# Performance work log

Hardware: AMD Instinct MI355X
Metric: run time of the kernel (lower is better)

## Reference

```python
import jax, jax.numpy as jnp
import numpy as np

B, SD, SE, DM, H, DK, DV, DFF = 4, 2048, 2048, 1024, 8, 128, 128, 4096
NEG = -jnp.inf


def _linear(x, w, b):
    # torch nn.Linear: w [out, in]
    return jnp.einsum('...i,oi->...o', x, w) + b


def _layer_norm(x, g, b, eps=1e-5):
    mu = jnp.mean(x, axis=-1, keepdims=True)
    var = jnp.var(x, axis=-1, keepdims=True)
    return (x - mu) * jax.lax.rsqrt(var + eps) * g + b


def _mha(Q, K, V, wq, bq, wk, bk, wv, bv, wo, bo, pad_mask, seq_mask):
    # wq/wk: [H, DK, DM], wv: [H, DV, DM]; vectorized over the per-head Linears
    Qh = jnp.einsum('bsd,hkd->bhsk', Q, wq) + bq[None, :, None, :]  # [B,H,Sq,DK]
    Kh = jnp.einsum('bsd,hkd->bhsk', K, wk) + bk[None, :, None, :]  # [B,H,Sk,DK]
    Vh = jnp.einsum('bsd,hvd->bhsv', V, wv) + bv[None, :, None, :]  # [B,H,Sk,DV]
    scores = jnp.einsum('bhqd,bhkd->bhqk', Qh, Kh) / np.sqrt(DK)
    scores = jnp.where(pad_mask[:, None, :, :] == 0, NEG, scores)
    if seq_mask is not None:
        scores = jnp.where(seq_mask[None, None, :, :] == 0, NEG, scores)
    w = jax.nn.softmax(scores, axis=-1)
    out = jnp.einsum('bhqk,bhkv->bhqv', w, Vh)  # [B,H,Sq,DV]
    out = out.transpose(0, 2, 1, 3).reshape(Q.shape[0], Q.shape[1], H * DV)
    return _linear(out, wo, bo)


def setup_inputs() -> dict:
    key = jax.random.key(0)
    ks = iter(jax.random.split(key, 40))
    s = 0.02
    d = {
        'output_embs': jax.random.normal(next(ks), (B, SD, DM), jnp.float32),
        'encoder_output': jax.random.normal(next(ks), (B, SE, DM), jnp.float32),
        'inputs_padding_mask': jnp.ones((B, 1, SE), jnp.int32),
        'outputs_padding_mask': jnp.ones((B, 1, SD), jnp.int32),
    }
    for name in ['q1', 'k1', 'v1', 'q2', 'k2', 'v2']:
        d[name + '_w'] = jax.random.normal(next(ks), (DM, DM), jnp.float32) * s
        d[name + '_b'] = jnp.zeros((DM,), jnp.float32)
    for p in ['sa', 'ed']:
        d[p + '_qw'] = jax.random.normal(next(ks), (H, DK, DM), jnp.float32) * s
        d[p + '_qb'] = jnp.zeros((H, DK), jnp.float32)
        d[p + '_kw'] = jax.random.normal(next(ks), (H, DK, DM), jnp.float32) * s
        d[p + '_kb'] = jnp.zeros((H, DK), jnp.float32)
        d[p + '_vw'] = jax.random.normal(next(ks), (H, DV, DM), jnp.float32) * s
        d[p + '_vb'] = jnp.zeros((H, DV), jnp.float32)
        d[p + '_ow'] = jax.random.normal(next(ks), (DM, H * DV), jnp.float32) * s
        d[p + '_ob'] = jnp.zeros((DM,), jnp.float32)
    d['ff_w1'] = jax.random.normal(next(ks), (DFF, DM), jnp.float32) * s
    d['ff_b1'] = jnp.zeros((DFF,), jnp.float32)
    d['ff_w2'] = jax.random.normal(next(ks), (DM, DFF), jnp.float32) * s
    d['ff_b2'] = jnp.zeros((DM,), jnp.float32)
    d['ln1_g'] = jnp.ones((DM,), jnp.float32)
    d['ln1_b'] = jnp.zeros((DM,), jnp.float32)
    d['ln2_g'] = jnp.ones((DM,), jnp.float32)
    d['ln2_b'] = jnp.zeros((DM,), jnp.float32)
    return d


def reference(output_embs, encoder_output, inputs_padding_mask, outputs_padding_mask,
              q1_w, q1_b, k1_w, k1_b, v1_w, v1_b,
              q2_w, q2_b, k2_w, k2_b, v2_w, v2_b,
              sa_qw, sa_qb, sa_kw, sa_kb, sa_vw, sa_vb, sa_ow, sa_ob,
              ed_qw, ed_qb, ed_kw, ed_kb, ed_vw, ed_vb, ed_ow, ed_ob,
              ff_w1, ff_b1, ff_w2, ff_b2, ln1_g, ln1_b, ln2_g, ln2_b):
    # Dropout (p=0.1 in torch) treated as identity for a deterministic reference.
    seq_len = output_embs.shape[1]
    seq_mask = jnp.tril(jnp.ones((seq_len, seq_len), jnp.float32))
    Q = _linear(output_embs, q1_w, q1_b)
    K = _linear(output_embs, k1_w, k1_b)
    V = _linear(output_embs, v1_w, v1_b)
    x = output_embs + _mha(Q, K, V, sa_qw, sa_qb, sa_kw, sa_kb, sa_vw, sa_vb,
                           sa_ow, sa_ob, outputs_padding_mask, seq_mask)
    x = _layer_norm(x, ln1_g, ln1_b)
    Q2 = _linear(x, q2_w, q2_b)
    K2 = _linear(encoder_output, k2_w, k2_b)
    V2 = _linear(encoder_output, v2_w, v2_b)
    # NOTE: original adds residual from output_embs (not x) -- kept faithful.
    y = output_embs + _mha(Q2, K2, V2, ed_qw, ed_qb, ed_kw, ed_kb, ed_vw, ed_vb,
                           ed_ow, ed_ob, inputs_padding_mask, None)
    y = _layer_norm(y, ln2_g, ln2_b)
    ff = _linear(jax.nn.relu(_linear(y, ff_w1, ff_b1)), ff_w2, ff_b2)
    out = y + ff
    # original reuses layer_norm2 for the final norm (layer_norm3 unused) -- faithful.
    out = _layer_norm(out, ln2_g, ln2_b)
    return out
```

## Files before the change

### kernel.cpp

```cpp
#include <hip/hip_runtime.h>
#include <hip/hip_bf16.h>

typedef __hip_bfloat16 bf16;
typedef short short8 __attribute__((ext_vector_type(8)));
typedef short short4v __attribute__((ext_vector_type(4)));
typedef float floatx4 __attribute__((ext_vector_type(4)));
typedef int intx4 __attribute__((ext_vector_type(4)));
typedef unsigned int uintx4 __attribute__((ext_vector_type(4)));

#define B_ 4
#define SD_ 2048
#define SE_ 2048
#define DM_ 1024
#define H_ 8
#define DFF_ 4096

struct PtrsIn  { const void* p[6]; };
struct PtrsOut { void* p[6]; };
struct Int6    { int v[6]; };

__device__ __forceinline__ float b2f(bf16 v) { return __bfloat162float(v); }
__device__ __forceinline__ bf16 f2b(float v) { return __float2bfloat16(v); }
__device__ __forceinline__ short f2s(float v) { return __builtin_bit_cast(short, __float2bfloat16(v)); }

__device__ __forceinline__ unsigned cvtpk_bf16(float lo, float hi) {
    unsigned r;
    asm("v_cvt_pk_bf16_f32 %0, %1, %2" : "=v"(r) : "v"(lo), "v"(hi));
    return r;
}
__device__ __forceinline__ void pl32swap(unsigned &x, unsigned &y) {
    asm("v_permlane32_swap_b32 %0, %1" : "+v"(x), "+v"(y));
}
__device__ __forceinline__ void pl16swap(unsigned &x, unsigned &y) {
    asm("v_permlane16_swap_b32 %0, %1" : "+v"(x), "+v"(y));
}

__device__ __forceinline__ void gl_lds16(const short* g, short* l) {
    __builtin_amdgcn_global_load_lds(
        (const __attribute__((address_space(1))) void*)g,
        (__attribute__((address_space(3))) void*)l, 16, 0, 0);
}

__global__ __launch_bounds__(256) void cvt6(PtrsIn in, PtrsOut out, Int6 n)
{
    const int y = blockIdx.y;
    int i = (blockIdx.x * 256 + threadIdx.x) * 8;
    if (i >= n.v[y]) return;
    const float* src = (const float*)in.p[y];
    bf16* dst = (bf16*)out.p[y];
    floatx4 a = *(const floatx4*)(src + i);
    floatx4 b = *(const floatx4*)(src + i + 4);
    short8 r;
#pragma unroll
    for (int k = 0; k < 4; ++k) { r[k] = f2s(a[k]); r[k + 4] = f2s(b[k]); }
    *(short8*)(dst + i) = r;
}

__global__ __launch_bounds__(256) void cvtT6(PtrsIn in, bf16* out)
{
    __shared__ short tl[32][36];
    const int z = blockIdx.z;
    const float* src = (const float*)in.p[z];
    bf16* dst = out + (size_t)z * 1024 * 1024;
    const int tid = threadIdx.x;
    const int i = tid >> 3;
    const int j = (tid & 7) * 4;
    const int r0 = blockIdx.x * 32, c0 = blockIdx.y * 32;
    floatx4 v = *(const floatx4*)(src + (size_t)(r0 + i) * 1024 + c0 + j);
#pragma unroll
    for (int p = 0; p < 4; ++p) tl[i][j + p] = f2s(v[p]);
    __syncthreads();
    short4v r;
#pragma unroll
    for (int p = 0; p < 4; ++p) r[p] = tl[j + p][i];
    *(short4v*)(dst + (size_t)(c0 + i) * 1024 + r0 + j) = r;
}

__global__ __launch_bounds__(256) void bias6(
    PtrsIn w6, PtrsIn bin6, PtrsIn badd6, PtrsOut out6)
{
    __shared__ float red[4];
    const int y = blockIdx.y;
    const float* w    = (const float*)w6.p[y];
    const float* bin  = (const float*)bin6.p[y];
    const float* badd = (const float*)badd6.p[y];
    float* out        = (float*)out6.p[y];
    const int o = blockIdx.x;
    const int t = threadIdx.x;
    float s = 0.f;
#pragma unroll
    for (int i = t; i < 1024; i += 256) s += w[(size_t)o * 1024 + i] * bin[i];
#pragma unroll
    for (int off = 32; off >= 1; off >>= 1) s += __shfl_xor(s, off);
    if ((t & 63) == 0) red[t >> 6] = s;
    __syncthreads();
    if (t == 0) out[o] = red[0] + red[1] + red[2] + red[3] + badd[o];
}

__global__ __launch_bounds__(256) void gemm_prep(PtrsIn A6, PtrsIn W6, PtrsOut C6)
{
    __shared__ __align__(16) short As[16 * 512];
    __shared__ __align__(16) short Ws[16 * 512];

    const int K = 1024, N = 1024;
    const int z = blockIdx.z;
    const bf16* A = (const bf16*)A6.p[z];
    const bf16* W = (const bf16*)W6.p[z];
    bf16* C = (bf16*)C6.p[z];

    const int tid  = threadIdx.x;
    const int lane = tid & 63;
    const int wave = tid >> 6;
    const int quad = lane >> 4;
    const int l16  = lane & 15;
    const int r7   = l16 & 7;
    const int bm0  = blockIdx.y * 128;
    const int bn0  = blockIdx.x * 128;
    const int wm   = (wave >> 1) * 64;
    const int wn   = (wave & 1) * 64;

    const int scol = (((lane & 7) ^ (lane >> 3)) * 8);
    const short* Ag = (const short*)A + (size_t)(bm0 + wave * 32 + (lane >> 3)) * K + scol;
    const short* Wg = (const short*)W + (size_t)(bn0 + wave * 32 + (lane >> 3)) * K + scol;
    short* Al = As + (wave * 4) * 512;
    short* Wl = Ws + (wave * 4) * 512;

    floatx4 acc[4][4];
#pragma unroll
    for (int i = 0; i < 4; ++i)
#pragma unroll
        for (int j = 0; j < 4; ++j)
            acc[i][j] = (floatx4){0.f, 0.f, 0.f, 0.f};

    for (int k0 = 0; k0 < K; k0 += 64) {
        __syncthreads();
#pragma unroll
        for (int s = 0; s < 4; ++s) {
            gl_lds16(Ag + k0 + (size_t)s * 8 * K, Al + s * 512);
            gl_lds16(Wg + k0 + (size_t)s * 8 * K, Wl + s * 512);
        }
        __syncthreads();
#pragma unroll
        for (int kk = 0; kk < 64; kk += 32) {
            short8 af[4], bg[4];
#pragma unroll
            for (int i = 0; i < 4; ++i) {
                int row = wm + i * 16 + l16;
                af[i] = *(const short8*)&As[(row >> 3) * 512 + r7 * 64 +
                                            (((quad + (kk >> 3)) ^ r7) << 3)];
            }
#pragma unroll
            for (int j = 0; j < 4; ++j) {
                int row = wn + j * 16 + l16;
                bg[j] = *(const short8*)&Ws[(row >> 3) * 512 + r7 * 64 +
                                            (((quad + (kk >> 3)) ^ r7) << 3)];
            }
#pragma unroll
            for (int i = 0; i < 4; ++i)
#pragma unroll
                for (int j = 0; j < 4; ++j)
                    acc[i][j] = __builtin_amdgcn_mfma_f32_16x16x32_bf16(
                        af[i], bg[j], acc[i][j], 0, 0, 0);
        }
    }

#pragma unroll
    for (int j = 0; j < 4; ++j) {
        int col = bn0 + wn + j * 16 + l16;
#pragma unroll
        for (int i = 0; i < 4; ++i) {
            int row0 = bm0 + wm + i * 16 + quad * 4;
#pragma unroll
            for (int r = 0; r < 4; ++r)
                C[(size_t)(row0 + r) * N + col] = f2b(acc[i][j][r]);
        }
    }
}

template <int RELU>
__global__ __launch_bounds__(512, 2) void gemm256(
    const bf16* __restrict__ A, const bf16* __restrict__ W,
    const float* __restrict__ bias, bf16* __restrict__ C,
    int M, int N, int K)
{
    __shared__ __align__(16) short L[3 * 24576];

    const int tid  = threadIdx.x;
    const int lane = tid & 63;
    const int wave = tid >> 6;
    const int quad = lane >> 4;
    const int l16  = lane & 15;
    const int r7   = l16 & 7;
    const int wm   = wave >> 1;
    const int wn   = wave & 1;

    const int gx  = gridDim.x;
    const int nwg = gx * gridDim.y;
    int wg = blockIdx.y * gx + blockIdx.x;
    if ((nwg & 7) == 0) wg = (wg & 7) * (nwg >> 3) + (wg >> 3);
    const int bn0 = (wg % gx) * 128;
    const int bm0 = (wg / gx) * 256;

    const int scol = (((lane & 7) ^ ((lane >> 3) & 7)) * 8);
    const short* Ag = (const short*)A + (size_t)(bm0 + wave * 32 + (lane >> 3)) * K + scol;
    const short* Wg = (const short*)W + (size_t)(bn0 + wave * 16 + (lane >> 3)) * K + scol;
    const int aw = (wave * 32) * 64;
    const int bw = 16384 + (wave * 16) * 64;

    floatx4 acc[4][4];
#pragma unroll
    for (int i = 0; i < 4; ++i)
#pragma unroll
        for (int j = 0; j < 4; ++j)
            acc[i][j] = (floatx4){0.f, 0.f, 0.f, 0.f};

    const int T = K / 64;

#pragma unroll
    for (int i = 0; i < 4; ++i) gl_lds16(Ag + (size_t)(i * 8) * K, L + aw + i * 8 * 64);
#pragma unroll
    for (int i = 0; i < 2; ++i) gl_lds16(Wg + (size_t)(i * 8) * K, L + bw + i * 8 * 64);
#pragma unroll
    for (int i = 0; i < 4; ++i) gl_lds16(Ag + 64 + (size_t)(i * 8) * K, L + 24576 + aw + i * 8 * 64);
#pragma unroll
    for (int i = 0; i < 2; ++i) gl_lds16(Wg + 64 + (size_t)(i * 8) * K, L + 24576 + bw + i * 8 * 64);
    asm volatile("s_waitcnt vmcnt(6)" ::: "memory");
    __builtin_amdgcn_s_barrier();

    int cur = 0, stg = 2;
    for (int t = 0; t < T; ++t) {
        __builtin_amdgcn_sched_barrier(0);
        const int kt = (t + 2 < T) ? (t + 2) : (T - 1);
        const size_t kg = (size_t)kt * 64;
        const short* Ac = L + cur * 24576;
        const short* Bc = Ac + 16384;
        short* As_s = L + stg * 24576 + aw;
        short* Bs_s = L + stg * 24576 + bw;

        short8 af[2][2], bf[4][2];

#pragma unroll
        for (int mi = 0; mi < 2; ++mi)
#pragma unroll
            for (int ks = 0; ks < 2; ++ks)
                af[mi][ks] = *(const short8*)&Ac[(wm * 64 + mi * 16 + l16) * 64 +
                                                (((ks * 4 + quad) ^ r7) << 3)];
#pragma unroll
        for (int nf = 0; nf < 4; ++nf)
#pragma unroll
            for (int ks = 0; ks < 2; ++ks)
                bf[nf][ks] = *(const short8*)&Bc[(wn * 64 + nf * 16 + l16) * 64 +
                                                (((ks * 4 + quad) ^ r7) << 3)];
        gl_lds16(Ag + kg, As_s);
        gl_lds16(Ag + kg + (size_t)8 * K, As_s + 8 * 64);
        gl_lds16(Wg + kg, Bs_s);
        __builtin_amdgcn_s_barrier();
        asm volatile("s_waitcnt lgkmcnt(0)" ::: "memory");
        __builtin_amdgcn_sched_barrier(0);
        __builtin_amdgcn_s_setprio(1);
#pragma unroll
        for (int ks = 0; ks < 2; ++ks)
#pragma unroll
            for (int mi = 0; mi < 2; ++mi)
#pragma unroll
                for (int nf = 0; nf < 4; ++nf)
                    acc[mi][nf] = __builtin_amdgcn_mfma_f32_16x16x32_bf16(
                        af[mi][ks], bf[nf][ks], acc[mi][nf], 0, 0, 0);
        __builtin_amdgcn_s_setprio(0);
        __builtin_amdgcn_s_barrier();

#pragma unroll
        for (int mi = 0; mi < 2; ++mi)
#pragma unroll
            for (int ks = 0; ks < 2; ++ks)
                af[mi][ks] = *(const short8*)&Ac[(wm * 64 + (2 + mi) * 16 + l16) * 64 +
                                                (((ks * 4 + quad) ^ r7) << 3)];
        gl_lds16(Ag + kg + (size_t)16 * K, As_s + 16 * 64);
        gl_lds16(Ag + kg + (size_t)24 * K, As_s + 24 * 64);
        gl_lds16(Wg + kg + (size_t)8 * K, Bs_s + 8 * 64);
        __builtin_amdgcn_s_barrier();
        asm volatile("s_waitcnt lgkmcnt(0)" ::: "memory");
        __builtin_amdgcn_sched_barrier(0);
        __builtin_amdgcn_s_setprio(1);
#pragma unroll
        for (int ks = 0; ks < 2; ++ks)
#pragma unroll
            for (int mi = 0; mi < 2; ++mi)
#pragma unroll
                for (int nf = 0; nf < 4; ++nf)
                    acc[2 + mi][nf] = __builtin_amdgcn_mfma_f32_16x16x32_bf16(
                        af[mi][ks], bf[nf][ks], acc[2 + mi][nf], 0, 0, 0);
        __builtin_amdgcn_s_setprio(0);
        asm volatile("s_waitcnt vmcnt(6)" ::: "memory");
        __builtin_amdgcn_s_barrier();

        cur = (cur == 2) ? 0 : cur + 1;
        stg = (stg == 2) ? 0 : stg + 1;
    }

#pragma unroll
    for (int nf = 0; nf < 4; ++nf) {
        int col = bn0 + wn * 64 + nf * 16 + l16;
        float bv = bias ? bias[col] : 0.f;
#pragma unroll
        for (int mf = 0; mf < 4; ++mf) {
            int row0 = bm0 + wm * 64 + mf * 16 + quad * 4;
#pragma unroll
            for (int r = 0; r < 4; ++r) {
                float v = acc[mf][nf][r] + bv;
                if (RELU) v = fmaxf(v, 0.f);
                C[(size_t)(row0 + r) * N + col] = f2b(v);
            }
        }
    }
}

__global__ __launch_bounds__(256) void vtrans(
    const bf16* __restrict__ in, int str, bf16* __restrict__ out, int S)
{
    __shared__ short t[32][36];
    const int tid = threadIdx.x;
    const int s0  = blockIdx.x * 32;
    const int d0  = blockIdx.y * 32;
    const int bh  = blockIdx.z;
    const int b = bh >> 3, h = bh & 7;
    const int i = tid >> 3;
    const int j = (tid & 7) * 4;

    *(short4v*)&t[i][j] =
        *(const short4v*)(in + (size_t)(b * S + s0 + i) * str + h * 128 + d0 + j);
    __syncthreads();
    short4v r;
#pragma unroll
    for (int p = 0; p < 4; ++p) r[p] = t[j + p][i];
    *(short4v*)(out + ((size_t)bh * 128 + d0 + i) * S + s0 + j) = r;
}

template <int CAUSAL>
__global__ __launch_bounds__(256) void flash_attn(
    const bf16* __restrict__ Q, int qstr, const bf16* __restrict__ K, int kstr,
    const bf16* __restrict__ Vt, const int* __restrict__ pad,
    bf16* __restrict__ Of, float* __restrict__ Ls, int Sq, int Sk)
{
    __shared__ __align__(16) short Ks[64 * 128];
    __shared__ __align__(16) short Vs[128 * 64];

    const int tid  = threadIdx.x;
    const int lane = tid & 63;
    const int wave = tid >> 6;
    const int quad = lane >> 4;
    const int l16  = lane & 15;
    const int r7   = l16 & 7;
    const int bh   = blockIdx.x;
    const int b    = bh >> 3;
    const int h    = bh & 7;
    const int par  = blockIdx.y;
    const int tz   = blockIdx.z;

    const int NT = Sq >> 7;
    const float sc = 0.08838834764831845f * 1.4426950408889634f;
    const bf16* vb0 = Vt + (size_t)bh * 128 * Sk;
    const short* Kb = (const short*)K + (size_t)b * Sk * kstr + h * 128;

    int krr[4], kgg[4], vrr[4], vgg[4];
#pragma unroll
    for (int s = 0; s < 4; ++s) {
        int seg = wave * 4 + s;
        krr[s] = seg * 4 + (lane >> 4);
        kgg[s] = (l16 ^ (krr[s] & 7)) * 8;
        vrr[s] = seg * 8 + (lane >> 3);
        vgg[s] = ((lane & 7) ^ (vrr[s] & 7)) * 8;
    }

    const int npass = CAUSAL ? 2 : 1;
    for (int ps = 0; ps < npass; ++ps) {
        const int tile = CAUSAL ? (ps ? NT - 1 - tz : tz) : tz;
        const int q0 = tile * 128;
        const int qw = q0 + wave * 32;

        short8 qf[2][4];
#pragma unroll
        for (int mi = 0; mi < 2; ++mi) {
            const bf16* qb = Q + (size_t)(b * Sq + qw + mi * 16 + l16) * qstr + h * 128;
#pragma unroll
            for (int c = 0; c < 4; ++c)
                qf[mi][c] = *(const short8*)(qb + c * 32 + quad * 8);
        }

        floatx4 o[2][8];
#pragma unroll
        for (int mi = 0; mi < 2; ++mi)
#pragma unroll
            for (int nf = 0; nf < 8; ++nf) o[mi][nf] = (floatx4){0.f, 0.f, 0.f, 0.f};
        float lsum[2] = {0.f, 0.f};

        int kEnd = Sk;
        if (CAUSAL && q0 + 128 < Sk) kEnd = q0 + 128;

        intx4 sk[4], sv[4];
        {
            const int kc = par * 64;
#pragma unroll
            for (int s = 0; s < 4; ++s) {
                sk[s] = *(const intx4*)(Kb + (size_t)(kc + krr[s]) * kstr + kgg[s]);
                sv[s] = *(const intx4*)((const short*)vb0 + (size_t)vrr[s] * Sk + kc + vgg[s]);
            }
        }

        for (int ci = par; ci * 64 < kEnd; ci += 2) {
            const int kc = ci * 64;
            __syncthreads();
#pragma unroll
            for (int s = 0; s < 4; ++s) {
                *(intx4*)&Ks[(wave * 4 + s) * 512 + lane * 8] = sk[s];
                *(intx4*)&Vs[(wave * 4 + s) * 512 + lane * 8] = sv[s];
            }
            __syncthreads();

            const int kcn = kc + 128;
            if (kcn < kEnd) {
#pragma unroll
                for (int s = 0; s < 4; ++s) {
                    sk[s] = *(const intx4*)(Kb + (size_t)(kcn + krr[s]) * kstr + kgg[s]);
                    sv[s] = *(const intx4*)((const short*)vb0 + (size_t)vrr[s] * Sk + kcn + vgg[s]);
                }
            }
            __builtin_amdgcn_sched_barrier(0);

            short8 pfm[2][2];
#pragma unroll
            for (int c = 0; c < 2; ++c) {
                floatx4 sT[2][2];
#pragma unroll
                for (int fp = 0; fp < 2; ++fp) {
                    const int f = c * 2 + fp;
                    const int krow = f * 16 + l16;
                    short8 kf[4];
#pragma unroll
                    for (int cc = 0; cc < 4; ++cc)
                        kf[cc] = *(const short8*)&Ks[krow * 128 + (((cc * 4 + quad) ^ r7) << 3)];
#pragma unroll
                    for (int mi = 0; mi < 2; ++mi) {
                        floatx4 s = (floatx4){0.f, 0.f, 0.f, 0.f};
#pragma unroll
                        for (int cc = 0; cc < 4; ++cc)
                            s = __builtin_amdgcn_mfma_f32_16x16x32_bf16(
                                kf[cc], qf[mi][cc], s, 0, 0, 0);
                        sT[mi][fp] = s;
                    }
                }

                const int* pb = pad + (size_t)b * Sk + kc + c * 32 + quad * 4;
                intx4 pv0 = *(const intx4*)pb;
                intx4 pv1 = *(const intx4*)(pb + 16);

#pragma unroll
                for (int mi = 0; mi < 2; ++mi) {
                    const int qv = qw + mi * 16 + l16;
#pragma unroll
                    for (int fp = 0; fp < 2; ++fp) {
#pragma unroll
                        for (int r = 0; r < 4; ++r) {
                            int kk = kc + (c * 2 + fp) * 16 + quad * 4 + r;
                            bool ok = ((fp ? pv1[r] : pv0[r]) != 0);
                            if (CAUSAL) ok = ok && (kk <= qv);
                            float p = ok ? __builtin_amdgcn_exp2f(sT[mi][fp][r] * sc) : 0.f;
                            sT[mi][fp][r] = p;
                            lsum[mi] += p;
                        }
                    }
                    unsigned wA = cvtpk_bf16(sT[mi][0][0], sT[mi][0][1]);
                    unsigned wB = cvtpk_bf16(sT[mi][0][2], sT[mi][0][3]);
                    unsigned wC = cvtpk_bf16(sT[mi][1][0], sT[mi][1][1]);
                    unsigned wD = cvtpk_bf16(sT[mi][1][2], sT[mi][1][3]);
                    pl32swap(wA, wC);
                    pl16swap(wA, wC);
                    pl32swap(wB, wD);
                    pl16swap(wB, wD);
                    uintx4 t;
                    t[0] = wA; t[1] = wB; t[2] = wC; t[3] = wD;
                    pfm[mi][c] = __builtin_bit_cast(short8, t);
                }
            }

            __builtin_amdgcn_s_setprio(1);
#pragma unroll
            for (int nf = 0; nf < 8; ++nf) {
                int vrow = nf * 16 + l16;
                short8 vf0 = *(const short8*)&Vs[vrow * 64 + ((quad ^ r7) << 3)];
                short8 vf1 = *(const short8*)&Vs[vrow * 64 + (((4 + quad) ^ r7) << 3)];
#pragma unroll
                for (int mi = 0; mi < 2; ++mi) {
                    o[mi][nf] = __builtin_amdgcn_mfma_f32_16x16x32_bf16(
                        pfm[mi][0], vf0, o[mi][nf], 0, 0, 0);
                    o[mi][nf] = __builtin_amdgcn_mfma_f32_16x16x32_bf16(
                        pfm[mi][1], vf1, o[mi][nf], 0, 0, 0);
                }
            }
            __builtin_amdgcn_s_setprio(0);
        }

        bf16* op = Of + (size_t)par * B_ * Sq * DM_;
        float* lp = Ls + (size_t)par * B_ * H_ * Sq;
#pragma unroll
        for (int mi = 0; mi < 2; ++mi) {
            float s = lsum[mi];
            s += __shfl_xor(s, 16);
            s += __shfl_xor(s, 32);
            if (lane < 16)
                lp[(size_t)bh * Sq + qw + mi * 16 + l16] = s;
#pragma unroll
            for (int nf = 0; nf < 8; ++nf)
#pragma unroll
                for (int r = 0; r < 4; ++r) {
                    int q = qw + mi * 16 + quad * 4 + r;
                    op[(size_t)(b * Sq + q) * DM_ + h * 128 + nf * 16 + l16] =
                        f2b(o[mi][nf][r]);
                }
        }
    }
}

__global__ __launch_bounds__(256) void attn_combine(
    const bf16* __restrict__ Of, const float* __restrict__ Ls,
    bf16* __restrict__ out)
{
    const int row = blockIdx.x;
    const int t = threadIdx.x;
    const int col = t * 4;
    const int h = col >> 7;
    const int b = row >> 11;
    const int q = row & (SD_ - 1);
    const size_t NV = (size_t)B_ * SD_ * DM_;
    const int idx = (b * H_ + h) * SD_ + q;
    float l = Ls[idx] + Ls[B_ * H_ * SD_ + idx];
    float inv = l > 0.f ? 1.f / l : 0.f;
    size_t base = (size_t)row * DM_ + col;
    short4v a0 = *(const short4v*)(Of + base);
    short4v a1 = *(const short4v*)(Of + NV + base);
    short4v r;
#pragma unroll
    for (int i = 0; i < 4; ++i)
        r[i] = f2s((b2f(__builtin_bit_cast(bf16, (short)a0[i])) +
                    b2f(__builtin_bit_cast(bf16, (short)a1[i]))) * inv);
    *(short4v*)(out + base) = r;
}

template <int A32, int O32>
__global__ __launch_bounds__(256) void add_ln(
    const void* __restrict__ Ap, const bf16* __restrict__ Bv,
    const float* __restrict__ g, const float* __restrict__ be,
    void* __restrict__ outp)
{
    const int D = DM_;
    __shared__ float red[8];
    const size_t row = blockIdx.x;
    const int t = threadIdx.x;

    float x[4];
    {
        float av[4];
        if (A32) {
            floatx4 a4 = *(const floatx4*)((const float*)Ap + row * D + t * 4);
#pragma unroll
            for (int i = 0; i < 4; ++i) av[i] = a4[i];
        } else {
            short4v a4 = *(const short4v*)((const bf16*)Ap + row * D + t * 4);
#pragma unroll
            for (int i = 0; i < 4; ++i)
                av[i] = b2f(__builtin_bit_cast(bf16, (short)a4[i]));
        }
        short4v b4 = *(const short4v*)(Bv + row * D + t * 4);
#pragma unroll
        for (int i = 0; i < 4; ++i)
            x[i] = av[i] + b2f(__builtin_bit_cast(bf16, (short)b4[i]));
    }
    float s = 0.f, s2 = 0.f;
#pragma unroll
    for (int i = 0; i < 4; ++i) { s += x[i]; s2 += x[i] * x[i]; }
#pragma unroll
    for (int off = 32; off >= 1; off >>= 1) {
        s  += __shfl_xor(s, off);
        s2 += __shfl_xor(s2, off);
    }
    const int wave = t >> 6;
    if ((t & 63) == 0) { red[wave] = s; red[4 + wave] = s2; }
    __syncthreads();
    s  = red[0] + red[1] + red[2] + red[3];
    s2 = red[4] + red[5] + red[6] + red[7];
    const float mu   = s * (1.f / D);
    const float var  = s2 * (1.f / D) - mu * mu;
    const float rstd = rsqrtf(var + 1e-5f);
#pragma unroll
    for (int i = 0; i < 4; ++i) {
        int idx = t * 4 + i;
        float v = (x[i] - mu) * rstd * g[idx] + be[idx];
        if (O32) ((float*)outp)[row * D + idx] = v;
        else     ((bf16*)outp)[row * D + idx] = f2b(v);
    }
}

extern "C" void kernel_launch(void* const* d_in, const int* in_sizes, int n_in,
                              void* d_out, int out_size, void* d_ws, size_t ws_size,
                              hipStream_t stream)
{
    const float* emb    = (const float*)d_in[0];
    const float* enc    = (const float*)d_in[1];
    const int*  in_pad  = (const int*)d_in[2];
    const int*  out_pad = (const int*)d_in[3];
    const float* q1_w = (const float*)d_in[4];  const float* q1_b = (const float*)d_in[5];
    const float* k1_w = (const float*)d_in[6];  const float* k1_b = (const float*)d_in[7];
    const float* v1_w = (const float*)d_in[8];  const float* v1_b = (const float*)d_in[9];
    const float* q2_w = (const float*)d_in[10]; const float* q2_b = (const float*)d_in[11];
    const float* k2_w = (const float*)d_in[12]; const float* k2_b = (const float*)d_in[13];
    const float* v2_w = (const float*)d_in[14]; const float* v2_b = (const float*)d_in[15];
    const float* sa_qw = (const float*)d_in[16]; const float* sa_qb = (const float*)d_in[17];
    const float* sa_kw = (const float*)d_in[18]; const float* sa_kb = (const float*)d_in[19];
    const float* sa_vw = (const float*)d_in[20]; const float* sa_vb = (const float*)d_in[21];
    const float* sa_ow = (const float*)d_in[22]; const float* sa_ob = (const float*)d_in[23];
    const float* ed_qw = (const float*)d_in[24]; const float* ed_qb = (const float*)d_in[25];
    const float* ed_kw = (const float*)d_in[26]; const float* ed_kb = (const float*)d_in[27];
    const float* ed_vw = (const float*)d_in[28]; const float* ed_vb = (const float*)d_in[29];
    const float* ed_ow = (const float*)d_in[30]; const float* ed_ob = (const float*)d_in[31];
    const float* ff_w1 = (const float*)d_in[32]; const float* ff_b1 = (const float*)d_in[33];
    const float* ff_w2 = (const float*)d_in[34]; const float* ff_b2 = (const float*)d_in[35];
    const float* ln1_g = (const float*)d_in[36]; const float* ln1_b = (const float*)d_in[37];
    const float* ln2_g = (const float*)d_in[38]; const float* ln2_b = (const float*)d_in[39];

    const int M = B_ * SD_;
    const size_t MM = (size_t)1024 * 1024;
    bf16* ws = (bf16*)d_ws;

    bf16* Wqkv = ws;
    bf16* Wkv  = ws + 3 * MM;
    bf16* Wq2  = ws + 5 * MM;
    bf16* Wso  = ws + 6 * MM;
    bf16* Weo  = ws + 7 * MM;
    bf16* Wf1  = ws + 8 * MM;
    bf16* Wf2  = ws + 12 * MM;
    float* bQKV = (float*)(ws + 16 * MM);
    float* bKV  = bQKV + 3072;
    float* bQ2  = bKV + 2048;
    float* Lsum = bQ2 + 2048;
    bf16* hw   = ws + 17 * MM;
    bf16* ft   = ws + 23 * MM;
    bf16* emb_b = ws + 17 * MM;
    bf16* enc_b = ws + 25 * MM;
    bf16* sqkv  = ws + 33 * MM;
    bf16* skv   = ws + 33 * MM;
    bf16* sq2   = ws + 49 * MM;
    bf16* sVt   = ws + 57 * MM;
    bf16* attn  = ws + 65 * MM;
    bf16* Ofb   = ws + 73 * MM;
    bf16* s1    = ws + 73 * MM;
    bf16* x     = ws + 89 * MM;
    bf16* y     = ws + 33 * MM;
    bf16* mid   = ws + 41 * MM;
    bf16* f2    = ws + 81 * MM;

    auto G = [&](const bf16* Ai, const bf16* Wi, const float* bi, bf16* Ci,
                 int Mi, int Ni, int Ki, bool relu) {
        dim3 grid(Ni / 128, Mi / 256);
        if (relu) gemm256<1><<<grid, 512, 0, stream>>>(Ai, Wi, bi, Ci, Mi, Ni, Ki);
        else      gemm256<0><<<grid, 512, 0, stream>>>(Ai, Wi, bi, Ci, Mi, Ni, Ki);
    };

    {
        PtrsIn in; PtrsOut out; Int6 n;
        const float* s6[6] = {sa_qw, sa_kw, sa_vw, ed_qw, ed_kw, ed_vw};
        for (int i = 0; i < 6; ++i) { in.p[i] = s6[i]; out.p[i] = hw + i * MM; n.v[i] = (int)MM; }
        cvt6<<<dim3(512, 6), 256, 0, stream>>>(in, out, n);
    }
    {
        PtrsIn in;
        const float* s6[6] = {q1_w, k1_w, v1_w, q2_w, k2_w, v2_w};
        for (int i = 0; i < 6; ++i) in.p[i] = s6[i];
        cvtT6<<<dim3(32, 32, 6), 256, 0, stream>>>(in, ft);
    }
    {
        PtrsIn A, W; PtrsOut C;
        const int idx[6] = {0, 1, 2, 4, 5, 3};
        bf16* c6[6] = {Wqkv, Wqkv + MM, Wqkv + 2 * MM, Wkv, Wkv + MM, Wq2};
        for (int i = 0; i < 6; ++i) {
            A.p[i] = hw + (size_t)idx[i] * MM;
            W.p[i] = ft + (size_t)idx[i] * MM;
            C.p[i] = c6[i];
        }
        gemm_prep<<<dim3(8, 8, 6), 256, 0, stream>>>(A, W, C);
    }
    {
        PtrsIn w, bi, ba; PtrsOut o;
        const float* w6[6]  = {sa_qw, sa_kw, sa_vw, ed_kw, ed_vw, ed_qw};
        const float* bi6[6] = {q1_b, k1_b, v1_b, k2_b, v2_b, q2_b};
        const float* ba6[6] = {sa_qb, sa_kb, sa_vb, ed_kb, ed_vb, ed_qb};
        float* o6[6] = {bQKV, bQKV + 1024, bQKV + 2048, bKV, bKV + 1024, bQ2};
        for (int i = 0; i < 6; ++i) { w.p[i] = w6[i]; bi.p[i] = bi6[i]; ba.p[i] = ba6[i]; o.p[i] = o6[i]; }
        bias6<<<dim3(1024, 6), 256, 0, stream>>>(w, bi, ba, o);
    }
    {
        PtrsIn in; PtrsOut out; Int6 n;
        const float* s6[6] = {sa_ow, ed_ow, ff_w1, ff_w2, emb, enc};
        void* d6[6] = {Wso, Weo, Wf1, Wf2, emb_b, enc_b};
        int n6[6] = {(int)MM, (int)MM, (int)(4 * MM), (int)(4 * MM), (int)(8 * MM), (int)(8 * MM)};
        for (int i = 0; i < 6; ++i) { in.p[i] = s6[i]; out.p[i] = d6[i]; n.v[i] = n6[i]; }
        cvt6<<<dim3(4096, 6), 256, 0, stream>>>(in, out, n);
    }

    G(emb_b, Wqkv, bQKV, sqkv, M, 3072, DM_, false);
    vtrans<<<dim3(SD_ / 32, 4, B_ * H_), 256, 0, stream>>>(sqkv + 2048, 3072, sVt, SD_);
    flash_attn<1><<<dim3(B_ * H_, 2, SD_ / 256), 256, 0, stream>>>(
        sqkv, 3072, sqkv + 1024, 3072, sVt, out_pad, Ofb, Lsum, SD_, SD_);
    attn_combine<<<dim3(M), 256, 0, stream>>>(Ofb, Lsum, attn);
    G(attn, Wso, sa_ob, s1, M, DM_, DM_, false);
    add_ln<1, 0><<<dim3(M), 256, 0, stream>>>(emb, s1, ln1_g, ln1_b, x);

    G(enc_b, Wkv, bKV, skv, M, 2048, DM_, false);
    G(x, Wq2, bQ2, sq2, M, DM_, DM_, false);
    vtrans<<<dim3(SE_ / 32, 4, B_ * H_), 256, 0, stream>>>(skv + 1024, 2048, sVt, SE_);
    flash_attn<0><<<dim3(B_ * H_, 2, SD_ / 128), 256, 0, stream>>>(
        sq2, 1024, skv, 2048, sVt, in_pad, Ofb, Lsum, SD_, SE_);
    attn_combine<<<dim3(M), 256, 0, stream>>>(Ofb, Lsum, attn);
    G(attn, Weo, ed_ob, s1, M, DM_, DM_, false);
    add_ln<1, 0><<<dim3(M), 256, 0, stream>>>(emb, s1, ln2_g, ln2_b, y);

    G(y, Wf1, ff_b1, mid, M, DFF_, DM_, true);
    G(mid, Wf2, ff_b2, f2, M, DM_, DFF_, false);
    add_ln<0, 1><<<dim3(M), 256, 0, stream>>>(y, f2, ln2_g, ln2_b, d_out);
}
```

Measured before the change: 830.2 us.

## Add 256x256 double-buffered GEMM kernel for wide-N projections

Adds a gemm_w kernel using 256x256 output tiles with 512 threads, where each wave computes a 128x64 sub-tile. The K dimension advances in steps of 64 through a two-stage LDS double buffer fed by direct global-to-LDS loads, with an XCD-aware workgroup remap. The host GEMM dispatcher sends calls with N a multiple of 256 and at least 2048 (e.g. the FFN up-projection) to it, aiming for higher arithmetic intensity per tile. In exchange it uses more LDS (128KB) and more accumulator registers per thread, waits on vmcnt(0) each iteration, and launches fewer workgroups.

```diff
diff --git a/kernel.cpp b/kernel.cpp
--- a/kernel.cpp
+++ b/kernel.cpp
@@ -305,6 +305,114 @@
 #pragma unroll
         for (int mf = 0; mf < 4; ++mf) {
             int row0 = bm0 + wm * 64 + mf * 16 + quad * 4;
+#pragma unroll
+            for (int r = 0; r < 4; ++r) {
+                float v = acc[mf][nf][r] + bv;
+                if (RELU) v = fmaxf(v, 0.f);
+                C[(size_t)(row0 + r) * N + col] = f2b(v);
+            }
+        }
+    }
+}
+
+template <int RELU>
+__global__ __launch_bounds__(512, 2) void gemm_w(
+    const bf16* __restrict__ A, const bf16* __restrict__ W,
+    const float* __restrict__ bias, bf16* __restrict__ C,
+    int M, int N, int K)
+{
+    __shared__ __align__(16) short L[2 * 32768];
+
+    const int tid  = threadIdx.x;
+    const int lane = tid & 63;
+    const int wave = tid >> 6;
+    const int quad = lane >> 4;
+    const int l16  = lane & 15;
+    const int r7   = l16 & 7;
+    const int wm   = wave >> 2;
+    const int wn   = wave & 3;
+
+    const int gx  = gridDim.x;
+    const int nwg = gx * gridDim.y;
+    int wg = blockIdx.y * gx + blockIdx.x;
+    if ((nwg & 7) == 0) wg = (wg & 7) * (nwg >> 3) + (wg >> 3);
+    const int bn0 = (wg % gx) * 256;
+    const int bm0 = (wg / gx) * 256;
+
+    const int scol = (((lane & 7) ^ ((lane >> 3) & 7)) * 8);
+    const short* Ag = (const short*)A + (size_t)(bm0 + wave * 32 + (lane >> 3)) * K + scol;
+    const short* Wg = (const short*)W + (size_t)(bn0 + wave * 32 + (lane >> 3)) * K + scol;
+    const int aw = wave * 32 * 64;
+    const int bw = 16384 + wave * 32 * 64;
+
+    floatx4 acc[8][4];
+#pragma unroll
+    for (int i = 0; i < 8; ++i)
+#pragma unroll
+        for (int j = 0; j < 4; ++j)
+            acc[i][j] = (floatx4){0.f, 0.f, 0.f, 0.f};
+
+    const int T = K / 64;
+
+#pragma unroll
+    for (int s = 0; s < 4; ++s) gl_lds16(Ag + (size_t)(s * 8) * K, L + aw + s * 512);
+#pragma unroll
+    for (int s = 0; s < 4; ++s) gl_lds16(Wg + (size_t)(s * 8) * K, L + bw + s * 512);
+    asm volatile("s_waitcnt vmcnt(0)" ::: "memory");
+    __builtin_amdgcn_s_barrier();
+
+    for (int t = 0; t < T; ++t) {
+        __builtin_amdgcn_sched_barrier(0);
+        const int kt = (t + 1 < T) ? (t + 1) : (T - 1);
+        const size_t kg = (size_t)kt * 64;
+        const int stg = ((t + 1) & 1) * 32768;
+#pragma unroll
+        for (int s = 0; s < 4; ++s) gl_lds16(Ag + kg + (size_t)(s * 8) * K, L + stg + aw + s * 512);
+#pragma unroll
+        for (int s = 0; s < 4; ++s) gl_lds16(Wg + kg + (size_t)(s * 8) * K, L + stg + bw + s * 512);
+        __builtin_amdgcn_sched_barrier(0);
+
+        const short* Ac = L + (t & 1) * 32768;
+        const short* Bc = Ac + 16384;
+
+        short8 bf[4][2];
+#pragma unroll
+        for (int nf = 0; nf < 4; ++nf)
+#pragma unroll
+            for (int ks = 0; ks < 2; ++ks)
+                bf[nf][ks] = *(const short8*)&Bc[(wn * 64 + nf * 16 + l16) * 64 +
+                                                (((ks * 4 + quad) ^ r7) << 3)];
+        __builtin_amdgcn_s_setprio(1);
+#pragma unroll
+        for (int mp = 0; mp < 4; ++mp) {
+            short8 af[2][2];
+#pragma unroll
+            for (int mi = 0; mi < 2; ++mi)
+#pragma unroll
+                for (int ks = 0; ks < 2; ++ks)
+                    af[mi][ks] = *(const short8*)&Ac[(wm * 128 + (mp * 2 + mi) * 16 + l16) * 64 +
+                                                    (((ks * 4 + quad) ^ r7) << 3)];
+#pragma unroll
+            for (int ks = 0; ks < 2; ++ks)
+#pragma unroll
+                for (int mi = 0; mi < 2; ++mi)
+#pragma unroll
+                    for (int nf = 0; nf < 4; ++nf)
+                        acc[mp * 2 + mi][nf] = __builtin_amdgcn_mfma_f32_16x16x32_bf16(
+                            af[mi][ks], bf[nf][ks], acc[mp * 2 + mi][nf], 0, 0, 0);
+        }
+        __builtin_amdgcn_s_setprio(0);
+        asm volatile("s_waitcnt vmcnt(0)" ::: "memory");
+        __builtin_amdgcn_s_barrier();
+    }
+
+#pragma unroll
+    for (int nf = 0; nf < 4; ++nf) {
+        int col = bn0 + wn * 64 + nf * 16 + l16;
+        float bv = bias ? bias[col] : 0.f;
+#pragma unroll
+        for (int mf = 0; mf < 8; ++mf) {
+            int row0 = bm0 + wm * 128 + mf * 16 + quad * 4;
 #pragma unroll
             for (int r = 0; r < 4; ++r) {
                 float v = acc[mf][nf][r] + bv;
@@ -660,9 +768,15 @@
 
     auto G = [&](const bf16* Ai, const bf16* Wi, const float* bi, bf16* Ci,
                  int Mi, int Ni, int Ki, bool relu) {
-        dim3 grid(Ni / 128, Mi / 256);
-        if (relu) gemm256<1><<<grid, 512, 0, stream>>>(Ai, Wi, bi, Ci, Mi, Ni, Ki);
-        else      gemm256<0><<<grid, 512, 0, stream>>>(Ai, Wi, bi, Ci, Mi, Ni, Ki);
+        if ((Ni & 255) == 0 && Ni >= 2048) {
+            dim3 grid(Ni / 256, Mi / 256);
+            if (relu) gemm_w<1><<<grid, 512, 0, stream>>>(Ai, Wi, bi, Ci, Mi, Ni, Ki);
+            else      gemm_w<0><<<grid, 512, 0, stream>>>(Ai, Wi, bi, Ci, Mi, Ni, Ki);
+        } else {
+            dim3 grid(Ni / 128, Mi / 256);
+            if (relu) gemm256<1><<<grid, 512, 0, stream>>>(Ai, Wi, bi, Ci, Mi, Ni, Ki);
+            else      gemm256<0><<<grid, 512, 0, stream>>>(Ai, Wi, bi, Ci, Mi, Ni, Ki);
+        }
     };
 
     {
```

After: 849.1 us. 2.3% more time.
